# Kernel tuning notes

Measured on AMD Instinct MI355X. Metric: run time of the kernel, lower is better.

The kernel has to match this reference:

```python
import jax, jax.numpy as jnp
import numpy as np

N_NODES = 50000
N_EDGES = 500000
D = 128
BN_EPS = 1e-5


def setup_inputs() -> dict:
    key = jax.random.key(0)
    ks = jax.random.split(key, 6)
    x = jax.random.normal(ks[0], (N_NODES, D), dtype=jnp.float32)
    edge_attr = jax.random.normal(ks[1], (N_EDGES, D), dtype=jnp.float32)
    edge_source = jax.random.randint(ks[2], (N_EDGES,), 0, N_NODES, dtype=jnp.int32)
    edge_target = jax.random.randint(ks[3], (N_EDGES,), 0, N_NODES, dtype=jnp.int32)
    # Linear weights stored as [in, out] = [3*D, D]; scaled like torch default init
    scale = 1.0 / np.sqrt(3 * D)
    Wf = jax.random.normal(ks[4], (3 * D, D), dtype=jnp.float32) * scale
    Ws = jax.random.normal(ks[5], (3 * D, D), dtype=jnp.float32) * scale
    bf = jnp.zeros((D,), dtype=jnp.float32)
    bs = jnp.zeros((D,), dtype=jnp.float32)
    gamma = jnp.ones((D,), dtype=jnp.float32)
    beta = jnp.zeros((D,), dtype=jnp.float32)
    return {"x": x, "edge_attr": edge_attr, "edge_source": edge_source,
            "edge_target": edge_target, "Wf": Wf, "bf": bf, "Ws": Ws, "bs": bs,
            "gamma": gamma, "beta": beta}


def reference(x, edge_attr, edge_source, edge_target, Wf, bf, Ws, bs, gamma, beta):
    # gather + concat: z is [E, 3*D]
    z = jnp.concatenate([x[edge_source], x[edge_target], edge_attr], axis=-1)
    # gated edge messages: sigmoid(linear_f(z)) * softplus(linear_s(z))  [E, D]
    msg = jax.nn.sigmoid(z @ Wf + bf) * jax.nn.softplus(z @ Ws + bs)
    # scatter-sum back to source nodes  [N, D]
    agg = jax.ops.segment_sum(msg, edge_source, num_segments=N_NODES)
    # BatchNorm1d (training mode: batch stats, biased variance)
    mean = jnp.mean(agg, axis=0)
    var = jnp.var(agg, axis=0)
    agg_bn = (agg - mean) * jax.lax.rsqrt(var + BN_EPS) * gamma + beta
    return jax.nn.softplus(x + agg_bn)
```

## Files before the change

### kernel.cpp

```cpp
#include <hip/hip_runtime.h>
#include <math.h>
#include <stdint.h>

#define N_NODES 50000
#define N_EDGES 500000
#define D 128
#define BE 64
#define KT 64
#define NKT 6
#define WROW 72
#define WSLAB (256 * WROW)
#define LOG2E 1.4426950408889634f
#define LN2   0.6931471805599453f

typedef __attribute__((ext_vector_type(8))) short bf16x8;
typedef __attribute__((ext_vector_type(4))) float floatx4;

__device__ __forceinline__ float fast_sigmoid(float v) {
    return __builtin_amdgcn_rcpf(1.0f + __builtin_amdgcn_exp2f(-v * LOG2E));
}
__device__ __forceinline__ float fast_softplus(float v) {
    float t = __builtin_amdgcn_exp2f(-fabsf(v) * LOG2E);
    return fmaxf(v, 0.0f) + __builtin_amdgcn_logf(1.0f + t) * LN2;
}
__device__ __forceinline__ uint32_t pack_bf16(float a, float b) {
    union { float f; uint32_t u; } ca, cb; ca.f = a; cb.f = b;
    return __builtin_amdgcn_perm(cb.u + 0x8000u, ca.u + 0x8000u, 0x07060302);
}

__global__ __launch_bounds__(256) void wt_prepass(
    const float* __restrict__ Wf, const float* __restrict__ Ws,
    unsigned short* __restrict__ Wt)
{
    const int n  = threadIdx.x;
    const int k0 = blockIdx.x * 16;
    const float* src = (n < 128) ? (Wf + n) : (Ws + (n - 128));
    unsigned short tmp[16];
#pragma unroll
    for (int j = 0; j < 16; j++) {
        union { float f; uint32_t u; } c; c.f = src[(size_t)(k0 + j) * D];
        tmp[j] = (unsigned short)((c.u + 0x8000u) >> 16);
    }
    const int kt = k0 >> 6;
    const int kk = k0 & 63;
    unsigned short* dst = Wt + (size_t)kt * WSLAB + (size_t)n * WROW + kk;
    *(uint4*)(dst)     = *(uint4*)(tmp);
    *(uint4*)(dst + 8) = *(uint4*)(tmp + 8);
    if (kk == 48) {
        uint4 z = {0, 0, 0, 0};
        *(uint4*)(dst + 16) = z;
    }
}

__global__ __launch_bounds__(256) void edge_msg_mfma(
    const float* __restrict__ x, const float* __restrict__ edge_attr,
    const int* __restrict__ esrc, const int* __restrict__ etgt,
    const unsigned short* __restrict__ Wt,
    const float* __restrict__ bfp, const float* __restrict__ bsp,
    float* __restrict__ agg)
{
    __shared__ unsigned short sW[WSLAB];
    __shared__ unsigned short sZ[BE * WROW];
    __shared__ int sSrc[BE];
    __shared__ int sTgt[BE];

    const int tid  = threadIdx.x;
    const int lane = tid & 63;
    const int w    = tid >> 6;
    const int e0   = blockIdx.x * BE;

    if (tid < BE) {
        sSrc[tid] = (e0 + tid < N_EDGES) ? esrc[e0 + tid] : 0;
    } else if (tid < 2 * BE) {
        int m = tid - BE;
        sTgt[m] = (e0 + m < N_EDGES) ? etgt[e0 + m] : 0;
    }
    __syncthreads();

    floatx4 acc[4][4];
#pragma unroll
    for (int mt = 0; mt < 4; mt++)
#pragma unroll
        for (int nt = 0; nt < 4; nt++) {
            floatx4 z = {0.f, 0.f, 0.f, 0.f};
            acc[mt][nt] = z;
        }

    const int zm = tid >> 2;
    const int zk = (tid & 3) * 16;

#pragma unroll 1
    for (int kt = 0; kt < NKT; kt++) {
        {
            const char* gbase = (const char*)(Wt + (size_t)kt * WSLAB) + w * 9216 + lane * 16;
            char* lbase = (char*)sW + w * 9216;
#pragma unroll
            for (int i = 0; i < 9; i++) {
                __builtin_amdgcn_global_load_lds(
                    (const __attribute__((address_space(1))) void*)(gbase + i * 1024),
                    (__attribute__((address_space(3))) void*)(lbase + i * 1024),
                    16, 0, 0);
            }
        }
        {
            const float* zsrc;
            int half = (kt & 1) * 64;
            if (kt < 2)      zsrc = x + (size_t)sSrc[zm] * D + half;
            else if (kt < 4) zsrc = x + (size_t)sTgt[zm] * D + half;
            else {
                int eg = e0 + zm;
                zsrc = edge_attr + (size_t)(eg < N_EDGES ? eg : 0) * D + half;
            }
            float4 f0 = *(const float4*)(zsrc + zk);
            float4 f1 = *(const float4*)(zsrc + zk + 4);
            float4 f2 = *(const float4*)(zsrc + zk + 8);
            float4 f3 = *(const float4*)(zsrc + zk + 12);
            uint4 lo, hi;
            lo.x = pack_bf16(f0.x, f0.y); lo.y = pack_bf16(f0.z, f0.w);
            lo.z = pack_bf16(f1.x, f1.y); lo.w = pack_bf16(f1.z, f1.w);
            hi.x = pack_bf16(f2.x, f2.y); hi.y = pack_bf16(f2.z, f2.w);
            hi.z = pack_bf16(f3.x, f3.y); hi.w = pack_bf16(f3.z, f3.w);
            uint32_t* dz = (uint32_t*)(sZ + (size_t)zm * WROW) + (zk >> 1);
            *(uint4*)(dz)     = lo;
            *(uint4*)(dz + 4) = hi;
        }
        __syncthreads();

#pragma unroll
        for (int ks = 0; ks < 2; ks++) {
            const int kb = ks * 32 + (lane >> 4) * 8;
            bf16x8 afr[4];
#pragma unroll
            for (int mt = 0; mt < 4; mt++)
                afr[mt] = *(const bf16x8*)(sZ + (mt * 16 + (lane & 15)) * WROW + kb);
            bf16x8 bfr[4];
#pragma unroll
            for (int nt = 0; nt < 4; nt++) {
                int n = (nt < 2) ? (w * 32 + nt * 16 + (lane & 15))
                                 : (128 + w * 32 + (nt - 2) * 16 + (lane & 15));
                bfr[nt] = *(const bf16x8*)(sW + n * WROW + kb);
            }
#pragma unroll
            for (int mt = 0; mt < 4; mt++)
#pragma unroll
                for (int nt = 0; nt < 4; nt++)
                    acc[mt][nt] = __builtin_amdgcn_mfma_f32_16x16x32_bf16(
                        afr[mt], bfr[nt], acc[mt][nt], 0, 0, 0);
        }
        __syncthreads();
    }

#pragma unroll
    for (int nt = 0; nt < 2; nt++) {
        const int col = w * 32 + nt * 16 + (lane & 15);
        const float bF = bfp[col];
        const float bS = bsp[col];
#pragma unroll
        for (int mt = 0; mt < 4; mt++) {
#pragma unroll
            for (int r = 0; r < 4; r++) {
                int mm = mt * 16 + (lane >> 4) * 4 + r;
                int eg = e0 + mm;
                if (eg >= N_EDGES) continue;
                float f = acc[mt][nt][r] + bF;
                float s = acc[mt][nt + 2][r] + bS;
                float msg = fast_sigmoid(f) * fast_softplus(s);
                atomicAdd(agg + (size_t)sSrc[mm] * D + col, msg);
            }
        }
    }
}

#define STATS_BLOCKS 128
__global__ __launch_bounds__(256) void bn_stats_kernel(
    const float* __restrict__ agg, float* __restrict__ stats)
{
    __shared__ float red[256];
    const int o    = threadIdx.x & (D - 1);
    const int half = threadIdx.x >> 7;
    const int rows = (N_NODES + STATS_BLOCKS - 1) / STATS_BLOCKS;
    int r0 = blockIdx.x * rows;
    int r1 = min(r0 + rows, N_NODES);
    float s = 0.0f, s2 = 0.0f;
    for (int r = r0 + half; r < r1; r += 2) {
        float v = agg[(size_t)r * D + o];
        s += v; s2 += v * v;
    }
    red[threadIdx.x] = s;
    __syncthreads();
    float stot = (threadIdx.x < 128) ? red[threadIdx.x] + red[threadIdx.x + 128] : 0.0f;
    __syncthreads();
    red[threadIdx.x] = s2;
    __syncthreads();
    if (threadIdx.x < 128) {
        float s2tot = red[threadIdx.x] + red[threadIdx.x + 128];
        atomicAdd(&stats[o], stot);
        atomicAdd(&stats[D + o], s2tot);
    }
}

__global__ __launch_bounds__(256) void bn_final_kernel(
    const float* __restrict__ x, const float* __restrict__ agg,
    const float* __restrict__ stats,
    const float* __restrict__ gamma, const float* __restrict__ beta,
    float* __restrict__ out)
{
    const int idx = blockIdx.x * blockDim.x + threadIdx.x;
    const int total4 = N_NODES * D / 4;
    if (idx >= total4) return;
    const int c4 = idx & (D / 4 - 1);
    const float inv_n = 1.0f / (float)N_NODES;

    float4 sm = *(const float4*)&stats[c4 * 4];
    float4 sq = *(const float4*)&stats[D + c4 * 4];
    float4 g  = *(const float4*)&gamma[c4 * 4];
    float4 b  = *(const float4*)&beta[c4 * 4];
    float4 xv = ((const float4*)x)[idx];
    float4 av = ((const float4*)agg)[idx];

    float4 o;
    {
        float mean = sm.x * inv_n, var = sq.x * inv_n - mean * mean;
        float is = rsqrtf(var + 1e-5f) * g.x;
        o.x = fast_softplus(xv.x + (av.x - mean) * is + b.x);
    }
    {
        float mean = sm.y * inv_n, var = sq.y * inv_n - mean * mean;
        float is = rsqrtf(var + 1e-5f) * g.y;
        o.y = fast_softplus(xv.y + (av.y - mean) * is + b.y);
    }
    {
        float mean = sm.z * inv_n, var = sq.z * inv_n - mean * mean;
        float is = rsqrtf(var + 1e-5f) * g.z;
        o.z = fast_softplus(xv.z + (av.z - mean) * is + b.z);
    }
    {
        float mean = sm.w * inv_n, var = sq.w * inv_n - mean * mean;
        float is = rsqrtf(var + 1e-5f) * g.w;
        o.w = fast_softplus(xv.w + (av.w - mean) * is + b.w);
    }
    ((float4*)out)[idx] = o;
}

extern "C" void kernel_launch(void* const* d_in, const int* in_sizes, int n_in,
                              void* d_out, int out_size, void* d_ws, size_t ws_size,
                              hipStream_t stream) {
    const float* x         = (const float*)d_in[0];
    const float* edge_attr = (const float*)d_in[1];
    const int*   esrc      = (const int*)d_in[2];
    const int*   etgt      = (const int*)d_in[3];
    const float* Wf        = (const float*)d_in[4];
    const float* bf_       = (const float*)d_in[5];
    const float* Ws        = (const float*)d_in[6];
    const float* bs_       = (const float*)d_in[7];
    const float* gamma     = (const float*)d_in[8];
    const float* beta      = (const float*)d_in[9];
    float* out = (float*)d_out;

    float* agg   = (float*)d_ws;
    float* stats = agg + (size_t)N_NODES * D;
    unsigned short* Wt = (unsigned short*)(stats + 2 * D);

    hipMemsetAsync(d_ws, 0, ((size_t)N_NODES * D + 2 * D) * sizeof(float), stream);

    wt_prepass<<<24, 256, 0, stream>>>(Wf, Ws, Wt);
    edge_msg_mfma<<<(N_EDGES + BE - 1) / BE, 256, 0, stream>>>(
        x, edge_attr, esrc, etgt, Wt, bf_, bs_, agg);
    bn_stats_kernel<<<STATS_BLOCKS, 256, 0, stream>>>(agg, stats);
    bn_final_kernel<<<(N_NODES * D / 4 + 255) / 256, 256, 0, stream>>>(
        x, agg, stats, gamma, beta, out);
}
```

Baseline: 693.6 us.

## Double the edge tile, register-prefetch next K slab, vectorize BN stats

```diff
diff --git a/kernel.cpp b/kernel.cpp
--- a/kernel.cpp
+++ b/kernel.cpp
@@ -5,8 +5,7 @@
 #define N_NODES 50000
 #define N_EDGES 500000
 #define D 128
-#define BE 64
-#define KT 64
+#define BE 128
 #define NKT 6
 #define WROW 72
 #define WSLAB (256 * WROW)
@@ -30,32 +29,28 @@
 
 __global__ __launch_bounds__(256) void wt_prepass(
     const float* __restrict__ Wf, const float* __restrict__ Ws,
-    unsigned short* __restrict__ Wt)
-{
+    uint4* __restrict__ Wt)
+{
+    const int kt = blockIdx.x >> 3;
+    const int i  = blockIdx.x & 7;
     const int n  = threadIdx.x;
-    const int k0 = blockIdx.x * 16;
     const float* src = (n < 128) ? (Wf + n) : (Ws + (n - 128));
-    unsigned short tmp[16];
-#pragma unroll
-    for (int j = 0; j < 16; j++) {
-        union { float f; uint32_t u; } c; c.f = src[(size_t)(k0 + j) * D];
-        tmp[j] = (unsigned short)((c.u + 0x8000u) >> 16);
-    }
-    const int kt = k0 >> 6;
-    const int kk = k0 & 63;
-    unsigned short* dst = Wt + (size_t)kt * WSLAB + (size_t)n * WROW + kk;
-    *(uint4*)(dst)     = *(uint4*)(tmp);
-    *(uint4*)(dst + 8) = *(uint4*)(tmp + 8);
-    if (kk == 48) {
-        uint4 z = {0, 0, 0, 0};
-        *(uint4*)(dst + 16) = z;
-    }
-}
-
-__global__ __launch_bounds__(256) void edge_msg_mfma(
+    const int k0 = kt * 64 + i * 8;
+    uint32_t u[4];
+#pragma unroll
+    for (int j = 0; j < 4; j++) {
+        float a = src[(size_t)(k0 + 2 * j) * D];
+        float b = src[(size_t)(k0 + 2 * j + 1) * D];
+        u[j] = pack_bf16(a, b);
+    }
+    uint4 v; v.x = u[0]; v.y = u[1]; v.z = u[2]; v.w = u[3];
+    Wt[(size_t)(kt * 8 + i) * 256 + n] = v;
+}
+
+__global__ __launch_bounds__(256, 2) void edge_msg_mfma(
     const float* __restrict__ x, const float* __restrict__ edge_attr,
     const int* __restrict__ esrc, const int* __restrict__ etgt,
-    const unsigned short* __restrict__ Wt,
+    const uint4* __restrict__ Wt,
     const float* __restrict__ bfp, const float* __restrict__ bsp,
     float* __restrict__ agg)
 {
@@ -69,70 +64,80 @@
     const int w    = tid >> 6;
     const int e0   = blockIdx.x * BE;
 
+    const int zm = tid >> 1;
+    const int zk = (tid & 1) * 32;
+
     if (tid < BE) {
         sSrc[tid] = (e0 + tid < N_EDGES) ? esrc[e0 + tid] : 0;
-    } else if (tid < 2 * BE) {
+    } else {
         int m = tid - BE;
         sTgt[m] = (e0 + m < N_EDGES) ? etgt[e0 + m] : 0;
     }
+
+    uint4 wreg[8];
+#pragma unroll
+    for (int i = 0; i < 8; i++) wreg[i] = Wt[(size_t)i * 256 + tid];
+
     __syncthreads();
 
-    floatx4 acc[4][4];
-#pragma unroll
-    for (int mt = 0; mt < 4; mt++)
+    float4 zreg[8];
+    {
+        const float* zsrc = x + (size_t)sSrc[zm] * D;
+#pragma unroll
+        for (int i = 0; i < 8; i++) zreg[i] = *(const float4*)(zsrc + zk + i * 4);
+    }
+
+    floatx4 acc[8][4];
+#pragma unroll
+    for (int mt = 0; mt < 8; mt++)
 #pragma unroll
         for (int nt = 0; nt < 4; nt++) {
             floatx4 z = {0.f, 0.f, 0.f, 0.f};
             acc[mt][nt] = z;
         }
 
-    const int zm = tid >> 2;
-    const int zk = (tid & 3) * 16;
-
-#pragma unroll 1
+#pragma unroll
     for (int kt = 0; kt < NKT; kt++) {
         {
-            const char* gbase = (const char*)(Wt + (size_t)kt * WSLAB) + w * 9216 + lane * 16;
-            char* lbase = (char*)sW + w * 9216;
-#pragma unroll
-            for (int i = 0; i < 9; i++) {
-                __builtin_amdgcn_global_load_lds(
-                    (const __attribute__((address_space(1))) void*)(gbase + i * 1024),
-                    (__attribute__((address_space(3))) void*)(lbase + i * 1024),
-                    16, 0, 0);
-            }
-        }
-        {
+            unsigned short* dw = sW + tid * WROW;
+#pragma unroll
+            for (int i = 0; i < 8; i++) *(uint4*)(dw + i * 8) = wreg[i];
+
+            uint32_t u[16];
+#pragma unroll
+            for (int i = 0; i < 8; i++) {
+                u[2 * i]     = pack_bf16(zreg[i].x, zreg[i].y);
+                u[2 * i + 1] = pack_bf16(zreg[i].z, zreg[i].w);
+            }
+            unsigned short* dz = sZ + zm * WROW + zk;
+#pragma unroll
+            for (int i = 0; i < 4; i++) {
+                uint4 v; v.x = u[4 * i]; v.y = u[4 * i + 1];
+                v.z = u[4 * i + 2]; v.w = u[4 * i + 3];
+                *(uint4*)(dz + i * 8) = v;
+            }
+        }
+        __syncthreads();
+
+        if (kt < NKT - 1) {
+            const int kn = kt + 1;
+#pragma unroll
+            for (int i = 0; i < 8; i++)
+                wreg[i] = Wt[(size_t)(kn * 8 + i) * 256 + tid];
             const float* zsrc;
-            int half = (kt & 1) * 64;
-            if (kt < 2)      zsrc = x + (size_t)sSrc[zm] * D + half;
-            else if (kt < 4) zsrc = x + (size_t)sTgt[zm] * D + half;
+            if (kn < 2)      zsrc = x + (size_t)sSrc[zm] * D + (kn & 1) * 64;
+            else if (kn < 4) zsrc = x + (size_t)sTgt[zm] * D + (kn & 1) * 64;
             else {
                 int eg = e0 + zm;
-                zsrc = edge_attr + (size_t)(eg < N_EDGES ? eg : 0) * D + half;
-            }
-            float4 f0 = *(const float4*)(zsrc + zk);
-            float4 f1 = *(const float4*)(zsrc + zk + 4);
-            float4 f2 = *(const float4*)(zsrc + zk + 8);
-            float4 f3 = *(const float4*)(zsrc + zk + 12);
-            uint4 lo, hi;
-            lo.x = pack_bf16(f0.x, f0.y); lo.y = pack_bf16(f0.z, f0.w);
-            lo.z = pack_bf16(f1.x, f1.y); lo.w = pack_bf16(f1.z, f1.w);
-            hi.x = pack_bf16(f2.x, f2.y); hi.y = pack_bf16(f2.z, f2.w);
-            hi.z = pack_bf16(f3.x, f3.y); hi.w = pack_bf16(f3.z, f3.w);
-            uint32_t* dz = (uint32_t*)(sZ + (size_t)zm * WROW) + (zk >> 1);
-            *(uint4*)(dz)     = lo;
-            *(uint4*)(dz + 4) = hi;
-        }
-        __syncthreads();
+                zsrc = edge_attr + (size_t)(eg < N_EDGES ? eg : 0) * D + (kn & 1) * 64;
+            }
+#pragma unroll
+            for (int i = 0; i < 8; i++) zreg[i] = *(const float4*)(zsrc + zk + i * 4);
+        }
 
 #pragma unroll
         for (int ks = 0; ks < 2; ks++) {
             const int kb = ks * 32 + (lane >> 4) * 8;
-            bf16x8 afr[4];
-#pragma unroll
-            for (int mt = 0; mt < 4; mt++)
-                afr[mt] = *(const bf16x8*)(sZ + (mt * 16 + (lane & 15)) * WROW + kb);
             bf16x8 bfr[4];
 #pragma unroll
             for (int nt = 0; nt < 4; nt++) {
@@ -141,11 +146,13 @@
                 bfr[nt] = *(const bf16x8*)(sW + n * WROW + kb);
             }
 #pragma unroll
-            for (int mt = 0; mt < 4; mt++)
+            for (int mt = 0; mt < 8; mt++) {
+                bf16x8 afr = *(const bf16x8*)(sZ + (mt * 16 + (lane & 15)) * WROW + kb);
 #pragma unroll
                 for (int nt = 0; nt < 4; nt++)
                     acc[mt][nt] = __builtin_amdgcn_mfma_f32_16x16x32_bf16(
-                        afr[mt], bfr[nt], acc[mt][nt], 0, 0, 0);
+                        afr, bfr[nt], acc[mt][nt], 0, 0, 0);
+            }
         }
         __syncthreads();
     }
@@ -156,7 +163,7 @@
         const float bF = bfp[col];
         const float bS = bsp[col];
 #pragma unroll
-        for (int mt = 0; mt < 4; mt++) {
+        for (int mt = 0; mt < 8; mt++) {
 #pragma unroll
             for (int r = 0; r < 4; r++) {
                 int mm = mt * 16 + (lane >> 4) * 4 + r;
@@ -175,27 +182,39 @@
 __global__ __launch_bounds__(256) void bn_stats_kernel(
     const float* __restrict__ agg, float* __restrict__ stats)
 {
-    __shared__ float red[256];
-    const int o    = threadIdx.x & (D - 1);
-    const int half = threadIdx.x >> 7;
+    __shared__ float4 redS[256];
+    __shared__ float4 redQ[256];
+    const int c4 = threadIdx.x & 31;
+    const int rg = threadIdx.x >> 5;
     const int rows = (N_NODES + STATS_BLOCKS - 1) / STATS_BLOCKS;
-    int r0 = blockIdx.x * rows;
-    int r1 = min(r0 + rows, N_NODES);
-    float s = 0.0f, s2 = 0.0f;
-    for (int r = r0 + half; r < r1; r += 2) {
-        float v = agg[(size_t)r * D + o];
-        s += v; s2 += v * v;
-    }
-    red[threadIdx.x] = s;
+    const int r0 = blockIdx.x * rows;
+    const int r1 = min(r0 + rows, N_NODES);
+    const float4* a4 = (const float4*)agg;
+
+    float4 s = {0, 0, 0, 0}, q = {0, 0, 0, 0};
+    for (int r = r0 + rg; r < r1; r += 8) {
+        float4 v = a4[(size_t)r * 32 + c4];
+        s.x += v.x; s.y += v.y; s.z += v.z; s.w += v.w;
+        q.x += v.x * v.x; q.y += v.y * v.y; q.z += v.z * v.z; q.w += v.w * v.w;
+    }
+    redS[threadIdx.x] = s;
+    redQ[threadIdx.x] = q;
     __syncthreads();
-    float stot = (threadIdx.x < 128) ? red[threadIdx.x] + red[threadIdx.x + 128] : 0.0f;
-    __syncthreads();
-    red[threadIdx.x] = s2;
-    __syncthreads();
-    if (threadIdx.x < 128) {
-        float s2tot = red[threadIdx.x] + red[threadIdx.x + 128];
-        atomicAdd(&stats[o], stot);
-        atomicAdd(&stats[D + o], s2tot);
+    if (rg == 0) {
+#pragma unroll
+        for (int j = 1; j < 8; j++) {
+            float4 ts = redS[c4 + j * 32], tq = redQ[c4 + j * 32];
+            s.x += ts.x; s.y += ts.y; s.z += ts.z; s.w += ts.w;
+            q.x += tq.x; q.y += tq.y; q.z += tq.z; q.w += tq.w;
+        }
+        atomicAdd(&stats[c4 * 4 + 0], s.x);
+        atomicAdd(&stats[c4 * 4 + 1], s.y);
+        atomicAdd(&stats[c4 * 4 + 2], s.z);
+        atomicAdd(&stats[c4 * 4 + 3], s.w);
+        atomicAdd(&stats[D + c4 * 4 + 0], q.x);
+        atomicAdd(&stats[D + c4 * 4 + 1], q.y);
+        atomicAdd(&stats[D + c4 * 4 + 2], q.z);
+        atomicAdd(&stats[D + c4 * 4 + 3], q.w);
     }
 }
 
@@ -259,11 +278,11 @@
 
     float* agg   = (float*)d_ws;
     float* stats = agg + (size_t)N_NODES * D;
-    unsigned short* Wt = (unsigned short*)(stats + 2 * D);
+    uint4* Wt    = (uint4*)(stats + 2 * D);
 
     hipMemsetAsync(d_ws, 0, ((size_t)N_NODES * D + 2 * D) * sizeof(float), stream);
 
-    wt_prepass<<<24, 256, 0, stream>>>(Wf, Ws, Wt);
+    wt_prepass<<<48, 256, 0, stream>>>(Wf, Ws, Wt);
     edge_msg_mfma<<<(N_EDGES + BE - 1) / BE, 256, 0, stream>>>(
         x, edge_attr, esrc, etgt, Wt, bf_, bs_, agg);
     bn_stats_kernel<<<STATS_BLOCKS, 256, 0, stream>>>(agg, stats);
```

Measured after the change: 888.0 us. +28.0%, slower.

## Replace atomic scatter with bf16 message buffer and CSR gather by source

Applied to the files above, without the earlier changes.

```diff
diff --git a/kernel.cpp b/kernel.cpp
--- a/kernel.cpp
+++ b/kernel.cpp
@@ -6,7 +6,6 @@
 #define N_EDGES 500000
 #define D 128
 #define BE 64
-#define KT 64
 #define NKT 6
 #define WROW 72
 #define WSLAB (256 * WROW)
@@ -27,29 +26,29 @@
     union { float f; uint32_t u; } ca, cb; ca.f = a; cb.f = b;
     return __builtin_amdgcn_perm(cb.u + 0x8000u, ca.u + 0x8000u, 0x07060302);
 }
+__device__ __forceinline__ unsigned short f2bf(float f) {
+    union { float f; uint32_t u; } c; c.f = f;
+    return (unsigned short)((c.u + 0x8000u) >> 16);
+}
 
 __global__ __launch_bounds__(256) void wt_prepass(
     const float* __restrict__ Wf, const float* __restrict__ Ws,
     unsigned short* __restrict__ Wt)
 {
+    const int kt = blockIdx.x >> 3;
+    const int i  = blockIdx.x & 7;
     const int n  = threadIdx.x;
-    const int k0 = blockIdx.x * 16;
     const float* src = (n < 128) ? (Wf + n) : (Ws + (n - 128));
-    unsigned short tmp[16];
-#pragma unroll
-    for (int j = 0; j < 16; j++) {
-        union { float f; uint32_t u; } c; c.f = src[(size_t)(k0 + j) * D];
-        tmp[j] = (unsigned short)((c.u + 0x8000u) >> 16);
-    }
-    const int kt = k0 >> 6;
-    const int kk = k0 & 63;
-    unsigned short* dst = Wt + (size_t)kt * WSLAB + (size_t)n * WROW + kk;
-    *(uint4*)(dst)     = *(uint4*)(tmp);
-    *(uint4*)(dst + 8) = *(uint4*)(tmp + 8);
-    if (kk == 48) {
-        uint4 z = {0, 0, 0, 0};
-        *(uint4*)(dst + 16) = z;
-    }
+    const int k0 = kt * 64 + i * 8;
+    uint32_t u[4];
+#pragma unroll
+    for (int j = 0; j < 4; j++) {
+        float a = src[(size_t)(k0 + 2 * j) * D];
+        float b = src[(size_t)(k0 + 2 * j + 1) * D];
+        u[j] = pack_bf16(a, b);
+    }
+    uint4 v; v.x = u[0]; v.y = u[1]; v.z = u[2]; v.w = u[3];
+    *(uint4*)(Wt + (size_t)(kt * 256 + n) * WROW + i * 8) = v;
 }
 
 __global__ __launch_bounds__(256) void edge_msg_mfma(
@@ -57,7 +56,7 @@
     const int* __restrict__ esrc, const int* __restrict__ etgt,
     const unsigned short* __restrict__ Wt,
     const float* __restrict__ bfp, const float* __restrict__ bsp,
-    float* __restrict__ agg)
+    float* __restrict__ agg, unsigned short* __restrict__ msgs, int mode)
 {
     __shared__ unsigned short sW[WSLAB];
     __shared__ unsigned short sZ[BE * WROW];
@@ -92,7 +91,7 @@
 #pragma unroll 1
     for (int kt = 0; kt < NKT; kt++) {
         {
-            const char* gbase = (const char*)(Wt + (size_t)kt * WSLAB) + w * 9216 + lane * 16;
+            const char* gbase = (const char*)Wt + (size_t)kt * 36864 + w * 9216 + lane * 16;
             char* lbase = (char*)sW + w * 9216;
 #pragma unroll
             for (int i = 0; i < 9; i++) {
@@ -165,37 +164,121 @@
                 float f = acc[mt][nt][r] + bF;
                 float s = acc[mt][nt + 2][r] + bS;
                 float msg = fast_sigmoid(f) * fast_softplus(s);
-                atomicAdd(agg + (size_t)sSrc[mm] * D + col, msg);
+                if (mode) {
+                    msgs[(size_t)eg * D + col] = f2bf(msg);
+                } else {
+                    atomicAdd(agg + (size_t)sSrc[mm] * D + col, msg);
+                }
             }
         }
     }
+}
+
+__global__ __launch_bounds__(512) void count_kernel(
+    const int* __restrict__ esrc, int* __restrict__ cnt)
+{
+    int e = blockIdx.x * 512 + threadIdx.x;
+    if (e < N_EDGES) atomicAdd(&cnt[esrc[e]], 1);
+}
+
+__global__ __launch_bounds__(1024) void scan_kernel(
+    const int* __restrict__ cnt, int* __restrict__ ofs)
+{
+    __shared__ int part[1024];
+    const int t = threadIdx.x;
+    const int CH = (N_NODES + 1023) / 1024;
+    const int i0 = t * CH;
+    int s = 0;
+    for (int j = 0; j < CH; j++) {
+        int i = i0 + j;
+        if (i < N_NODES) s += cnt[i];
+    }
+    part[t] = s;
+    __syncthreads();
+    for (int off = 1; off < 1024; off <<= 1) {
+        int v = (t >= off) ? part[t - off] : 0;
+        __syncthreads();
+        part[t] += v;
+        __syncthreads();
+    }
+    int running = part[t] - s;
+    for (int j = 0; j < CH; j++) {
+        int i = i0 + j;
+        if (i < N_NODES) { ofs[i] = running; running += cnt[i]; }
+    }
+}
+
+__global__ __launch_bounds__(512) void fill_kernel(
+    const int* __restrict__ esrc, int* __restrict__ ofs, int* __restrict__ eidx)
+{
+    int e = blockIdx.x * 512 + threadIdx.x;
+    if (e < N_EDGES) {
+        int slot = atomicAdd(&ofs[esrc[e]], 1);
+        eidx[slot] = e;
+    }
+}
+
+__global__ __launch_bounds__(512) void gather_kernel(
+    const unsigned short* __restrict__ msgs, const int* __restrict__ eidx,
+    const int* __restrict__ cnt, const int* __restrict__ ofs,
+    float* __restrict__ agg)
+{
+    const int lane = threadIdx.x & 63;
+    const int w    = threadIdx.x >> 6;
+    const int n    = blockIdx.x * 8 + w;
+    if (n >= N_NODES) return;
+    const int deg  = cnt[n];
+    const int base = ofs[n] - deg;
+    float a0 = 0.0f, a1 = 0.0f;
+    for (int j = 0; j < deg; j++) {
+        int id = eidx[base + j];
+        uint32_t p = *(const uint32_t*)(msgs + (size_t)id * D + 2 * lane);
+        union { uint32_t u; float f; } c0, c1;
+        c0.u = p << 16;
+        c1.u = p & 0xFFFF0000u;
+        a0 += c0.f; a1 += c1.f;
+    }
+    float2 o; o.x = a0; o.y = a1;
+    *(float2*)(agg + (size_t)n * D + 2 * lane) = o;
 }
 
 #define STATS_BLOCKS 128
 __global__ __launch_bounds__(256) void bn_stats_kernel(
     const float* __restrict__ agg, float* __restrict__ stats)
 {
-    __shared__ float red[256];
-    const int o    = threadIdx.x & (D - 1);
-    const int half = threadIdx.x >> 7;
+    __shared__ float4 redS[256];
+    __shared__ float4 redQ[256];
+    const int c4 = threadIdx.x & 31;
+    const int rg = threadIdx.x >> 5;
     const int rows = (N_NODES + STATS_BLOCKS - 1) / STATS_BLOCKS;
-    int r0 = blockIdx.x * rows;
-    int r1 = min(r0 + rows, N_NODES);
-    float s = 0.0f, s2 = 0.0f;
-    for (int r = r0 + half; r < r1; r += 2) {
-        float v = agg[(size_t)r * D + o];
-        s += v; s2 += v * v;
-    }
-    red[threadIdx.x] = s;
+    const int r0 = blockIdx.x * rows;
+    const int r1 = min(r0 + rows, N_NODES);
+    const float4* a4 = (const float4*)agg;
+
+    float4 s = {0, 0, 0, 0}, q = {0, 0, 0, 0};
+    for (int r = r0 + rg; r < r1; r += 8) {
+        float4 v = a4[(size_t)r * 32 + c4];
+        s.x += v.x; s.y += v.y; s.z += v.z; s.w += v.w;
+        q.x += v.x * v.x; q.y += v.y * v.y; q.z += v.z * v.z; q.w += v.w * v.w;
+    }
+    redS[threadIdx.x] = s;
+    redQ[threadIdx.x] = q;
     __syncthreads();
-    float stot = (threadIdx.x < 128) ? red[threadIdx.x] + red[threadIdx.x + 128] : 0.0f;
-    __syncthreads();
-    red[threadIdx.x] = s2;
-    __syncthreads();
-    if (threadIdx.x < 128) {
-        float s2tot = red[threadIdx.x] + red[threadIdx.x + 128];
-        atomicAdd(&stats[o], stot);
-        atomicAdd(&stats[D + o], s2tot);
+    if (rg == 0) {
+#pragma unroll
+        for (int j = 1; j < 8; j++) {
+            float4 ts = redS[c4 + j * 32], tq = redQ[c4 + j * 32];
+            s.x += ts.x; s.y += ts.y; s.z += ts.z; s.w += ts.w;
+            q.x += tq.x; q.y += tq.y; q.z += tq.z; q.w += tq.w;
+        }
+        atomicAdd(&stats[c4 * 4 + 0], s.x);
+        atomicAdd(&stats[c4 * 4 + 1], s.y);
+        atomicAdd(&stats[c4 * 4 + 2], s.z);
+        atomicAdd(&stats[c4 * 4 + 3], s.w);
+        atomicAdd(&stats[D + c4 * 4 + 0], q.x);
+        atomicAdd(&stats[D + c4 * 4 + 1], q.y);
+        atomicAdd(&stats[D + c4 * 4 + 2], q.z);
+        atomicAdd(&stats[D + c4 * 4 + 3], q.w);
     }
 }
 
@@ -259,13 +342,28 @@
 
     float* agg   = (float*)d_ws;
     float* stats = agg + (size_t)N_NODES * D;
-    unsigned short* Wt = (unsigned short*)(stats + 2 * D);
-
-    hipMemsetAsync(d_ws, 0, ((size_t)N_NODES * D + 2 * D) * sizeof(float), stream);
-
-    wt_prepass<<<24, 256, 0, stream>>>(Wf, Ws, Wt);
-    edge_msg_mfma<<<(N_EDGES + BE - 1) / BE, 256, 0, stream>>>(
-        x, edge_attr, esrc, etgt, Wt, bf_, bs_, agg);
+    int*   cnt   = (int*)(stats + 2 * D);
+    int*   ofs   = cnt + N_NODES;
+    unsigned short* Wt = (unsigned short*)(ofs + N_NODES);
+    int*   eidx  = (int*)((char*)Wt + 221184);
+    unsigned short* msgs = (unsigned short*)(eidx + N_EDGES);
+    const size_t NEED = 25600000ULL + 1024 + 400000 + 221184 + 2000000 + 128000000ULL;
+    const int mode = (ws_size >= NEED) ? 1 : 0;
+
+    wt_prepass<<<48, 256, 0, stream>>>(Wf, Ws, Wt);
+    if (mode) {
+        hipMemsetAsync(stats, 0, 1024 + 200000, stream);
+        edge_msg_mfma<<<(N_EDGES + BE - 1) / BE, 256, 0, stream>>>(
+            x, edge_attr, esrc, etgt, Wt, bf_, bs_, agg, msgs, 1);
+        count_kernel<<<(N_EDGES + 511) / 512, 512, 0, stream>>>(esrc, cnt);
+        scan_kernel<<<1, 1024, 0, stream>>>(cnt, ofs);
+        fill_kernel<<<(N_EDGES + 511) / 512, 512, 0, stream>>>(esrc, ofs, eidx);
+        gather_kernel<<<(N_NODES + 7) / 8, 512, 0, stream>>>(msgs, eidx, cnt, ofs, agg);
+    } else {
+        hipMemsetAsync(d_ws, 0, ((size_t)N_NODES * D + 2 * D) * sizeof(float), stream);
+        edge_msg_mfma<<<(N_EDGES + BE - 1) / BE, 256, 0, stream>>>(
+            x, edge_attr, esrc, etgt, Wt, bf_, bs_, agg, msgs, 0);
+    }
     bn_stats_kernel<<<STATS_BLOCKS, 256, 0, stream>>>(agg, stats);
     bn_final_kernel<<<(N_NODES * D / 4 + 255) / 256, 256, 0, stream>>>(
         x, agg, stats, gamma, beta, out);
```

Result: slower. 784.3 us (+13.1%).
